# Kernel tuning notes

Hardware: AMD Instinct MI355X
Metric: run time of the kernel (lower is better)

Reference implementation:

```python
import jax, jax.numpy as jnp
import numpy as np

B, S, D = 4, 2048, 1024

def setup_inputs() -> dict:
    key = jax.random.key(0)
    kv, kk, kq, kw = jax.random.split(key, 4)
    scale = 1.0 / np.sqrt(D)
    v = jax.random.normal(kv, (B, S, D), dtype=jnp.float32)
    k = jax.random.normal(kk, (B, S, D), dtype=jnp.float32)
    q = jax.random.normal(kq, (B, S, D), dtype=jnp.float32)
    wi = jax.random.normal(kw, (D, D), dtype=jnp.float32) * scale
    mask = jnp.tril(jnp.ones((S, S), dtype=bool))[None, :, :]  # causal [1,S,S]
    return {"v": v, "k": k, "q": q, "wi": wi, "mask": mask}

def reference(v, k, q, wi, mask):
    # project q, k, v with the shared weight wi
    q = q @ wi
    k = k @ wi
    v = v @ wi
    # scaled dot-product scores [B,S,S]
    scores = jnp.einsum('bqd,bkd->bqk', q, k) / jnp.sqrt(jnp.asarray(q.shape[-1], q.dtype))
    scores = jnp.where(mask, scores, jnp.asarray(-1e10, scores.dtype))
    attn = jax.nn.softmax(scores, axis=-1)
    # residual: q + attn @ v
    return q + jnp.einsum('bqk,bkd->bqd', attn, v)
```

## Files before the change

### kernel.cpp

```cpp
#include <hip/hip_runtime.h>
#include <hip/hip_bf16.h>

typedef __hip_bfloat16 bf16;
typedef short bf16x8 __attribute__((ext_vector_type(8)));
typedef float f32x4 __attribute__((ext_vector_type(4)));

#define HT 16384

__device__ __forceinline__ void gload16(const void* g, void* l) {
    __builtin_amdgcn_global_load_lds(
        (const __attribute__((address_space(1))) void*)g,
        (__attribute__((address_space(3))) void*)l, 16, 0, 0);
}

__device__ __forceinline__ void stage_half(char* lds, const bf16* src, int ld,
                                           int rowbase, int k0, int slotIdx,
                                           int tid)
{
    char* dst = lds + (size_t)slotIdx * HT + tid * 16;
    const int sub = tid >> 3;
    const int cb  = ((tid & 7) ^ (sub & 7)) << 4;
    #pragma unroll
    for (int p = 0; p < 2; ++p) {
        const int row = p * 64 + sub;
        const char* g = (const char*)(src + (size_t)(rowbase + row) * ld + k0) + cb;
        gload16(g, dst + p * 8192);
    }
}

__device__ __forceinline__ void stage_q(char* lds, const bf16* src, int ld,
                                        int rowbase, int k0, int slotIdx,
                                        int tid)
{
    char* dst = lds + (size_t)slotIdx * HT + tid * 16;
    #pragma unroll
    for (int p = 0; p < 4; ++p) {
        const int s = p * 256 + tid;
        const int row = s >> 3;
        const int cb = ((s & 7) ^ (row & 7)) << 4;
        const char* g = (const char*)(src + (size_t)(rowbase + row) * ld + k0) + cb;
        gload16(g, dst + p * 4096);
    }
}

__device__ __forceinline__ bf16x8 ldsfrag(const char* lds, int slotIdx,
                                          int row, int ks, int cb0)
{
    return *(const bf16x8*)(lds + (size_t)slotIdx * HT
                            + row * 128 + (cb0 ^ (ks << 6)));
}

__device__ __forceinline__ float bf2f(short s) {
    union { float f; unsigned u; } c;
    c.u = ((unsigned)(unsigned short)s) << 16;
    return c.f;
}

#define MF8(n0)                                                               \
    _Pragma("unroll") for (int m = 0; m < 4; ++m)                             \
    _Pragma("unroll") for (int dn = 0; dn < 2; ++dn)                          \
    _Pragma("unroll") for (int ks = 0; ks < 2; ++ks)                          \
        acc[m][(n0)+dn] = __builtin_amdgcn_mfma_f32_16x16x32_bf16(            \
            af[m][ks], bv[(n0)+dn][ks], acc[m][(n0)+dn], 0, 0, 0);

#define GEMM256_BODY(A_, lda_, B_, ldb_, brow_, bcol_)                        \
    f32x4 acc[4][4] = {};                                                     \
    bf16x8 af[4][2], bv[4][2];                                                \
    stage_half(lds, A_, lda_, brow_,       0, 0, tid);                        \
    stage_half(lds, A_, lda_, brow_ + 128, 0, 1, tid);                        \
    stage_half(lds, B_, ldb_, bcol_,       0, 6, tid);                        \
    stage_half(lds, A_, lda_, brow_,      64, 2, tid);                        \
    stage_half(lds, A_, lda_, brow_ + 128,64, 3, tid);                        \
    stage_half(lds, B_, ldb_, bcol_,     64, 7, tid);                         \
    asm volatile("s_waitcnt vmcnt(6)" ::: "memory");                          \
    __builtin_amdgcn_s_barrier();                                             \
    for (int t = 0; t < 16; ++t) {                                            \
        const int aslot = (t % 3) * 2 + hA;                                   \
        const int bslot = 6 + (t & 1);                                        \
        const int a2    = ((t + 2) % 3) * 2;                                  \
        const int k2    = min(t + 2, 15) << 6;                                \
        _Pragma("unroll") for (int m = 0; m < 4; ++m)                         \
        _Pragma("unroll") for (int ks = 0; ks < 2; ++ks)                      \
            af[m][ks] = ldsfrag(lds, aslot, rA + m * 16 + fr, ks, cb0);       \
        _Pragma("unroll") for (int n = 0; n < 4; ++n)                         \
        _Pragma("unroll") for (int ks = 0; ks < 2; ++ks)                      \
            bv[n][ks] = ldsfrag(lds, bslot, rB + n * 16 + fr, ks, cb0);       \
        stage_half(lds, A_, lda_, brow_,       k2, a2,     tid);              \
        stage_half(lds, A_, lda_, brow_ + 128, k2, a2 + 1, tid);              \
        __builtin_amdgcn_s_barrier();                                         \
        __builtin_amdgcn_s_setprio(1);                                        \
        MF8(0)                                                                \
        __builtin_amdgcn_s_setprio(0);                                        \
        __builtin_amdgcn_s_barrier();                                         \
        stage_half(lds, B_, ldb_, bcol_, k2, bslot, tid);                     \
        __builtin_amdgcn_s_barrier();                                         \
        __builtin_amdgcn_s_setprio(1);                                        \
        MF8(2)                                                                \
        __builtin_amdgcn_s_setprio(0);                                        \
        asm volatile("s_waitcnt vmcnt(6)" ::: "memory");                      \
        __builtin_amdgcn_s_barrier();                                         \
    }

template<int MODE>
__launch_bounds__(512, 2)
__global__ void gemm_a256(const bf16* __restrict__ A, const bf16* __restrict__ B,
                          bf16* __restrict__ Cb, float* __restrict__ Cf)
{
    extern __shared__ char lds[];
    const int gx = gridDim.x;
    const int nwg = gx * gridDim.y;
    const int chunk = nwg >> 3;
    const int orig = blockIdx.y * gx + blockIdx.x;
    const int wk2 = (orig & 7) * chunk + (orig >> 3);
    const int bi = wk2 / gx, bj = wk2 % gx;
    const int brow = bi * 256, bcol = bj * 128;

    const int tid  = threadIdx.x;
    const int lane = tid & 63;
    const int w    = tid >> 6;
    const int wm   = w >> 1, wn = w & 1;
    const int fr   = lane & 15, fq = lane >> 4;
    const int cb0  = ((fr & 7) ^ fq) << 4;
    const int hA   = wm >> 1;
    const int rA   = (wm & 1) * 64;
    const int rB   = wn * 64;

    GEMM256_BODY(A, 1024, B, 1024, brow, bcol)

    #pragma unroll
    for (int mf = 0; mf < 4; ++mf) {
        const int r0 = brow + wm * 64 + mf * 16 + fq * 4;
        #pragma unroll
        for (int nf = 0; nf < 4; ++nf) {
            const int c = bcol + wn * 64 + nf * 16 + fr;
            #pragma unroll
            for (int j = 0; j < 4; ++j) {
                if (MODE == 0)
                    Cb[(size_t)(r0 + j) * 1024 + c] =
                        __float2bfloat16(acc[mf][nf][j]);
                else
                    Cf[(size_t)(r0 + j) * 1024 + c] = acc[mf][nf][j];
            }
        }
    }
}

__launch_bounds__(512, 1)
__global__ void scores8(const bf16* __restrict__ qG, const bf16* __restrict__ kb,
                        bf16* __restrict__ P)
{
    extern __shared__ char lds[];
    const int orig = blockIdx.y * 8 + blockIdx.x;
    const int wk2 = (orig & 7) * 18 + (orig >> 3);
    const int bz = wk2 / 36;
    const int j  = wk2 % 36;
    int bi = (int)((__fsqrt_rn(8.0f * j + 1.0f) - 1.0f) * 0.5f);
    while ((bi + 1) * (bi + 2) / 2 <= j) ++bi;
    while (bi * (bi + 1) / 2 > j) --bi;
    const int bj = j - bi * (bi + 1) / 2;
    const int brow = bi * 256, bcol = bj * 256;
    const bf16* A = qG + (size_t)bz * 2048 * 1024;
    const bf16* B = kb + (size_t)bz * 2048 * 1024;
    bf16* Cp = P + (size_t)bz * 2048 * 2048;

    const int tid  = threadIdx.x;
    const int lane = tid & 63;
    const int w    = tid >> 6;
    const int wm   = w >> 2;
    const int wn   = w & 3;
    const int bh   = wn >> 1;
    const int rBl  = (wn & 1) * 64;
    const int fr   = lane & 15, fq = lane >> 4;
    const int cb0  = ((fr & 7) ^ fq) << 4;

    f32x4 acc[8][4] = {};
    bf16x8 af0[4][2], af1[4][2], bv0[2][2], bv1[2][2];

#define AS(t,h) ((((t) % 3) * 2) + (h))
#define BS(t,h) (6 + (((t) & 1) * 2) + (h))

    stage_half(lds, A, 1024, brow,       0, AS(0,0), tid);
    stage_half(lds, A, 1024, brow + 128, 0, AS(0,1), tid);
    stage_half(lds, B, 1024, bcol,       0, BS(0,0), tid);
    stage_half(lds, B, 1024, bcol + 128, 0, BS(0,1), tid);
    stage_half(lds, A, 1024, brow,      64, AS(1,0), tid);
    stage_half(lds, A, 1024, brow + 128,64, AS(1,1), tid);
    stage_half(lds, B, 1024, bcol,     64, BS(1,0), tid);
    asm volatile("s_waitcnt vmcnt(6)" ::: "memory");
    __builtin_amdgcn_s_barrier();

#define MFQ(MH, NH, AF, BV)                                                   \
    _Pragma("unroll") for (int m = 0; m < 4; ++m)                             \
    _Pragma("unroll") for (int n = 0; n < 2; ++n)                             \
    _Pragma("unroll") for (int ks = 0; ks < 2; ++ks)                          \
        acc[(MH)*4+m][(NH)*2+n] = __builtin_amdgcn_mfma_f32_16x16x32_bf16(    \
            AF[m][ks], BV[n][ks], acc[(MH)*4+m][(NH)*2+n], 0, 0, 0);

    for (int t = 0; t < 16; ++t) {
        const int kN  = min(t + 1, 15) << 6;
        const int kNN = min(t + 2, 15) << 6;
        const int as  = AS(t, wm);
        const int bs2 = BS(t, bh);

        #pragma unroll
        for (int m = 0; m < 4; ++m)
            #pragma unroll
            for (int ks = 0; ks < 2; ++ks)
                af0[m][ks] = ldsfrag(lds, as, m * 16 + fr, ks, cb0);
        #pragma unroll
        for (int n = 0; n < 2; ++n)
            #pragma unroll
            for (int ks = 0; ks < 2; ++ks)
                bv0[n][ks] = ldsfrag(lds, bs2, rBl + n * 16 + fr, ks, cb0);
        stage_half(lds, B, 1024, bcol + 128, kN, BS(t + 1, 1), tid);
        __builtin_amdgcn_s_barrier();
        __builtin_amdgcn_s_setprio(1);
        MFQ(0, 0, af0, bv0)
        __builtin_amdgcn_s_setprio(0);
        __builtin_amdgcn_s_barrier();

        #pragma unroll
        for (int m = 0; m < 4; ++m)
            #pragma unroll
            for (int ks = 0; ks < 2; ++ks)
                af1[m][ks] = ldsfrag(lds, as, 64 + m * 16 + fr, ks, cb0);
        stage_half(lds, A, 1024, brow, kNN, AS(t + 2, 0), tid);
        __builtin_amdgcn_s_barrier();
        __builtin_amdgcn_s_setprio(1);
        MFQ(1, 0, af1, bv0)
        __builtin_amdgcn_s_setprio(0);
        __builtin_amdgcn_s_barrier();

        #pragma unroll
        for (int n = 0; n < 2; ++n)
            #pragma unroll
            for (int ks = 0; ks < 2; ++ks)
                bv1[n][ks] = ldsfrag(lds, bs2, rBl + 32 + n * 16 + fr, ks, cb0);
        stage_half(lds, A, 1024, brow + 128, kNN, AS(t + 2, 1), tid);
        __builtin_amdgcn_s_barrier();
        __builtin_amdgcn_s_setprio(1);
        MFQ(1, 1, af1, bv1)
        __builtin_amdgcn_s_setprio(0);
        __builtin_amdgcn_s_barrier();

        stage_half(lds, B, 1024, bcol, kNN, BS(t + 2, 0), tid);
        __builtin_amdgcn_s_barrier();
        __builtin_amdgcn_s_setprio(1);
        MFQ(0, 1, af0, bv1)
        __builtin_amdgcn_s_setprio(0);
        asm volatile("s_waitcnt vmcnt(6)" ::: "memory");
        __builtin_amdgcn_s_barrier();
    }
#undef MFQ
#undef AS
#undef BS

    #pragma unroll
    for (int mf = 0; mf < 8; ++mf) {
        const int r0 = brow + wm * 128 + mf * 16 + fq * 4;
        #pragma unroll
        for (int nf = 0; nf < 4; ++nf) {
            const int c = bcol + wn * 64 + nf * 16 + fr;
            #pragma unroll
            for (int jj = 0; jj < 4; ++jj)
                Cp[(size_t)(r0 + jj) * 2048 + c] =
                    __float2bfloat16(acc[mf][nf][jj] * 0.03125f);
        }
    }
}

__device__ __forceinline__ void tile128pv(char* lds, const bf16* A, const bf16* B,
                                          bf16* Cb, const bf16* Res,
                                          int lda, int ldb, int ldcb,
                                          int brow, int bcol, int NT, int tid)
{
    const int lane = tid & 63;
    const int w    = tid >> 6;
    const int wm   = w >> 1, wn = w & 1;
    const int fr   = lane & 15, fq = lane >> 4;
    const int cb0  = ((fr & 7) ^ fq) << 4;

    f32x4 acc[4][4] = {};
    bf16x8 af[4][2], bv[4][2];

    stage_q(lds, A, lda, brow, 0,  0, tid);
    stage_q(lds, B, ldb, bcol, 0,  3, tid);
    stage_q(lds, A, lda, brow, 64, 1, tid);
    stage_q(lds, B, ldb, bcol, 64, 4, tid);
    asm volatile("s_waitcnt vmcnt(8)" ::: "memory");
    __builtin_amdgcn_s_barrier();

    for (int t = 0; t < NT; ++t) {
        const int aslot = t % 3, bslot = 3 + (t & 1);
        const int k2 = min(t + 2, NT - 1) << 6;

        #pragma unroll
        for (int m = 0; m < 4; ++m)
            #pragma unroll
            for (int ks = 0; ks < 2; ++ks)
                af[m][ks] = ldsfrag(lds, aslot, wm * 64 + m * 16 + fr, ks, cb0);
        #pragma unroll
        for (int n = 0; n < 4; ++n)
            #pragma unroll
            for (int ks = 0; ks < 2; ++ks)
                bv[n][ks] = ldsfrag(lds, bslot, wn * 64 + n * 16 + fr, ks, cb0);
        stage_q(lds, A, lda, brow, k2, (t + 2) % 3, tid);
        __builtin_amdgcn_s_barrier();
        __builtin_amdgcn_s_setprio(1);
        #pragma unroll
        for (int m = 0; m < 4; ++m)
            #pragma unroll
            for (int n = 0; n < 2; ++n)
                #pragma unroll
                for (int ks = 0; ks < 2; ++ks)
                    acc[m][n] = __builtin_amdgcn_mfma_f32_16x16x32_bf16(
                        af[m][ks], bv[n][ks], acc[m][n], 0, 0, 0);
        __builtin_amdgcn_s_setprio(0);
        __builtin_amdgcn_s_barrier();

        stage_q(lds, B, ldb, bcol, k2, bslot, tid);
        __builtin_amdgcn_s_barrier();
        __builtin_amdgcn_s_setprio(1);
        #pragma unroll
        for (int m = 0; m < 4; ++m)
            #pragma unroll
            for (int n = 2; n < 4; ++n)
                #pragma unroll
                for (int ks = 0; ks < 2; ++ks)
                    acc[m][n] = __builtin_amdgcn_mfma_f32_16x16x32_bf16(
                        af[m][ks], bv[n][ks], acc[m][n], 0, 0, 0);
        __builtin_amdgcn_s_setprio(0);
        asm volatile("s_waitcnt vmcnt(8)" ::: "memory");
        __builtin_amdgcn_s_barrier();
    }

    #pragma unroll
    for (int mf = 0; mf < 4; ++mf) {
        const int r0 = brow + wm * 64 + mf * 16 + fq * 4;
        #pragma unroll
        for (int nf = 0; nf < 4; ++nf) {
            const int c = bcol + wn * 64 + nf * 16 + fr;
            #pragma unroll
            for (int j = 0; j < 4; ++j)
                Cb[(size_t)(r0 + j) * ldcb + c] = __float2bfloat16(
                    acc[mf][nf][j] +
                    __bfloat162float(Res[(size_t)(r0 + j) * ldcb + c]));
        }
    }
}

__launch_bounds__(256, 2)
__global__ void pv128(const bf16* __restrict__ P, const bf16* __restrict__ vT,
                      const bf16* __restrict__ qb, bf16* __restrict__ Y)
{
    extern __shared__ char lds[];
    const int x  = blockIdx.x;
    const int u  = x & 255;
    const int bs = u & 7;
    const int bj = (u >> 3) & 7;
    const int bz = u >> 6;
    const int bi = (x >> 8) ? (15 - bs) : bs;

    tile128pv(lds,
              P + (size_t)bz * 2048 * 2048,
              vT + (size_t)bz * 1024 * 2048,
              Y + (size_t)bz * 2048 * 1024,
              qb + (size_t)bz * 2048 * 1024,
              2048, 2048, 1024,
              bi * 128, bj * 128, 2 * (bi + 1), threadIdx.x);
}

__device__ __forceinline__ void tr64(const float* __restrict__ src, int ldsrc,
                                     bf16* __restrict__ dst, int lddst,
                                     int r0, int c0, int tid, bf16* tl)
{
    #pragma unroll
    for (int p = 0; p < 4; ++p) {
        const int rr = p * 16 + (tid >> 4);
        const int cc = (tid & 15) * 4;
        float4 x = *(const float4*)(src + (size_t)(r0 + rr) * ldsrc + c0 + cc);
        bf16* o = tl + rr * 66 + cc;
        o[0] = __float2bfloat16(x.x);
        o[1] = __float2bfloat16(x.y);
        o[2] = __float2bfloat16(x.z);
        o[3] = __float2bfloat16(x.w);
    }
    __syncthreads();
    #pragma unroll
    for (int p = 0; p < 2; ++p) {
        const int crow = p * 32 + (tid >> 3);
        const int sc   = (tid & 7) * 8;
        union { short h[8]; bf16x8 v8; } o;
        #pragma unroll
        for (int j = 0; j < 8; ++j) {
            bf16 hh = tl[(sc + j) * 66 + crow];
            o.h[j] = *(short*)&hh;
        }
        *(bf16x8*)(dst + (size_t)(c0 + crow) * lddst + r0 + sc) = o.v8;
    }
}

__global__ void prep(const float* __restrict__ q, const float* __restrict__ k,
                     const float* __restrict__ wi, const float* __restrict__ v,
                     bf16* __restrict__ qb, bf16* __restrict__ kb,
                     bf16* __restrict__ Wb, bf16* __restrict__ vT,
                     bf16* __restrict__ Wt)
{
    __shared__ bf16 tl[64 * 66];
    const int b = blockIdx.x;
    const int tid = threadIdx.x;
    if (b < 2048) {
        const int z = b >> 9, rem = b & 511;
        const int d0 = (rem >> 5) * 64, s0 = (rem & 31) * 64;
        tr64(v + (size_t)z * 2048 * 1024, 1024,
             vT + (size_t)z * 1024 * 2048, 2048, s0, d0, tid, tl);
    } else if (b < 2304) {
        const int t2 = b - 2048;
        const int n0 = (t2 & 15) * 64, k0 = (t2 >> 4) * 64;
        tr64(wi, 1024, Wt, 1024, k0, n0, tid, tl);
    } else {
        const int N8 = 8192 * 1024 / 8, W8 = 1024 * 1024 / 8;
        const int total = 2 * N8 + W8;
        const int nconv = gridDim.x - 2304;
        for (int i = (b - 2304) * 256 + tid; i < total; i += nconv * 256) {
            const float4* s;
            bf16* dst;
            int j;
            if (i < N8)          { s = (const float4*)q;  dst = qb; j = i; }
            else if (i < 2 * N8) { s = (const float4*)k;  dst = kb; j = i - N8; }
            else                 { s = (const float4*)wi; dst = Wb; j = i - 2 * N8; }
            float4 a = s[2 * j], bb = s[2 * j + 1];
            float vals[8] = {a.x, a.y, a.z, a.w, bb.x, bb.y, bb.z, bb.w};
            union { short h[8]; bf16x8 v8; } o;
            #pragma unroll
            for (int e = 0; e < 8; ++e) {
                bf16 hh = __float2bfloat16(vals[e]);
                o.h[e] = *(short*)&hh;
            }
            ((bf16x8*)dst)[j] = o.v8;
        }
    }
}

__launch_bounds__(256)
__global__ void softmax_rows(bf16* __restrict__ P)
{
    const int wid = threadIdx.x >> 6, lane = threadIdx.x & 63;
    const int r = blockIdx.x * 4 + wid, b = blockIdx.y;
    bf16* row = P + ((size_t)b * 2048 + r) * 2048;
    const int nv  = r + 1;
    const int rup = (r & ~127) + 128;

    float vals[4][8];
    float m = -1e30f;
    #pragma unroll
    for (int c = 0; c < 4; ++c) {
        const int k0 = c * 512 + lane * 8;
        if (k0 < rup) {
            bf16x8 x = *(const bf16x8*)(row + k0);
            #pragma unroll
            for (int j = 0; j < 8; ++j) {
                float f = (k0 + j < nv) ? bf2f(x[j]) : -1e30f;
                vals[c][j] = f;
                m = fmaxf(m, f);
            }
        } else {
            #pragma unroll
            for (int j = 0; j < 8; ++j) vals[c][j] = -1e30f;
        }
    }
    #pragma unroll
    for (int o = 32; o; o >>= 1) m = fmaxf(m, __shfl_xor(m, o));

    float sum = 0.f;
    #pragma unroll
    for (int c = 0; c < 4; ++c)
        #pragma unroll
        for (int j = 0; j < 8; ++j) {
            float e = __expf(vals[c][j] - m);
            vals[c][j] = e;
            sum += e;
        }
    #pragma unroll
    for (int o = 32; o; o >>= 1) sum += __shfl_xor(sum, o);
    const float inv = 1.0f / sum;

    #pragma unroll
    for (int c = 0; c < 4; ++c) {
        const int k0 = c * 512 + lane * 8;
        if (k0 < rup) {
            union { short h[8]; bf16x8 v8; } o;
            #pragma unroll
            for (int j = 0; j < 8; ++j) {
                bf16 hh = __float2bfloat16(vals[c][j] * inv);
                o.h[j] = *(short*)&hh;
            }
            *(bf16x8*)(row + k0) = o.v8;
        }
    }
}

extern "C" void kernel_launch(void* const* d_in, const int* in_sizes, int n_in,
                              void* d_out, int out_size, void* d_ws, size_t ws_size,
                              hipStream_t stream)
{
    const float* v  = (const float*)d_in[0];
    const float* k  = (const float*)d_in[1];
    const float* q  = (const float*)d_in[2];
    const float* wi = (const float*)d_in[3];
    float* out = (float*)d_out;

    char* ws = (char*)d_ws;
    const size_t MB = 1u << 20;
    bf16* Wb = (bf16*)(ws);
    bf16* Wt = (bf16*)(ws + 2 * MB);
    bf16* G  = (bf16*)(ws + 4 * MB);
    bf16* qb = (bf16*)(ws + 6 * MB);
    bf16* kb = (bf16*)(ws + 22 * MB);
    bf16* vT = (bf16*)(ws + 38 * MB);
    bf16* qG = (bf16*)(ws + 54 * MB);
    bf16* Y  = (bf16*)(ws + 70 * MB);
    bf16* P  = (bf16*)(ws + 86 * MB);

    (void)hipFuncSetAttribute((const void*)gemm_a256<0>,
            hipFuncAttributeMaxDynamicSharedMemorySize, 131072);
    (void)hipFuncSetAttribute((const void*)gemm_a256<2>,
            hipFuncAttributeMaxDynamicSharedMemorySize, 131072);
    (void)hipFuncSetAttribute((const void*)scores8,
            hipFuncAttributeMaxDynamicSharedMemorySize, 163840);
    (void)hipFuncSetAttribute((const void*)pv128,
            hipFuncAttributeMaxDynamicSharedMemorySize, 81920);

    prep<<<5376, 256, 0, stream>>>(q, k, wi, v, qb, kb, Wb, vT, Wt);

    gemm_a256<0><<<dim3(8, 4), 512, 131072, stream>>>(Wb, Wb, G, nullptr);

    gemm_a256<0><<<dim3(8, 32), 512, 131072, stream>>>(qb, G, qG, nullptr);

    scores8<<<dim3(8, 18), 512, 163840, stream>>>(qG, kb, P);

    softmax_rows<<<dim3(512, 4), 256, 0, stream>>>(P);

    pv128<<<dim3(512), 256, 81920, stream>>>(P, vT, qb, Y);

    gemm_a256<2><<<dim3(8, 32), 512, 131072, stream>>>(Y, Wt, nullptr, out);
}
```

Before: 160.9 us.

## Store transposed V in contiguous 128x64 tiles for PV staging

```diff
diff --git a/kernel.cpp b/kernel.cpp
--- a/kernel.cpp
+++ b/kernel.cpp
@@ -39,6 +39,21 @@
         const int row = s >> 3;
         const int cb = ((s & 7) ^ (row & 7)) << 4;
         const char* g = (const char*)(src + (size_t)(rowbase + row) * ld + k0) + cb;
+        gload16(g, dst + p * 4096);
+    }
+}
+
+__device__ __forceinline__ void stage_qt(char* lds, const bf16* vtz,
+                                         int bcol, int k0, int slotIdx, int tid)
+{
+    const bf16* tile = vtz + ((size_t)(bcol >> 7) * 32 + (k0 >> 6)) * 8192;
+    char* dst = lds + (size_t)slotIdx * HT + tid * 16;
+    #pragma unroll
+    for (int p = 0; p < 4; ++p) {
+        const int s = p * 256 + tid;
+        const int row = s >> 3;
+        const int cb = ((s & 7) ^ (row & 7)) << 4;
+        const char* g = (const char*)(tile + row * 64) + cb;
         gload16(g, dst + p * 4096);
     }
 }
@@ -269,9 +284,10 @@
     }
 }
 
-__device__ __forceinline__ void tile128pv(char* lds, const bf16* A, const bf16* B,
+__device__ __forceinline__ void tile128pv(char* lds, const bf16* A,
+                                          const bf16* vtz,
                                           bf16* Cb, const bf16* Res,
-                                          int lda, int ldb, int ldcb,
+                                          int lda, int ldcb,
                                           int brow, int bcol, int NT, int tid)
 {
     const int lane = tid & 63;
@@ -284,9 +300,9 @@
     bf16x8 af[4][2], bv[4][2];
 
     stage_q(lds, A, lda, brow, 0,  0, tid);
-    stage_q(lds, B, ldb, bcol, 0,  3, tid);
+    stage_qt(lds, vtz, bcol, 0,  3, tid);
     stage_q(lds, A, lda, brow, 64, 1, tid);
-    stage_q(lds, B, ldb, bcol, 64, 4, tid);
+    stage_qt(lds, vtz, bcol, 64, 4, tid);
     asm volatile("s_waitcnt vmcnt(8)" ::: "memory");
     __builtin_amdgcn_s_barrier();
 
@@ -318,7 +334,7 @@
         __builtin_amdgcn_s_setprio(0);
         __builtin_amdgcn_s_barrier();
 
-        stage_q(lds, B, ldb, bcol, k2, bslot, tid);
+        stage_qt(lds, vtz, bcol, k2, bslot, tid);
         __builtin_amdgcn_s_barrier();
         __builtin_amdgcn_s_setprio(1);
         #pragma unroll
@@ -363,10 +379,10 @@
 
     tile128pv(lds,
               P + (size_t)bz * 2048 * 2048,
-              vT + (size_t)bz * 1024 * 2048,
+              vT + (size_t)bz * 8 * 32 * 8192,
               Y + (size_t)bz * 2048 * 1024,
               qb + (size_t)bz * 2048 * 1024,
-              2048, 2048, 1024,
+              2048, 1024,
               bi * 128, bj * 128, 2 * (bi + 1), threadIdx.x);
 }
 
@@ -406,23 +422,50 @@
                      bf16* __restrict__ Wb, bf16* __restrict__ vT,
                      bf16* __restrict__ Wt)
 {
-    __shared__ bf16 tl[64 * 66];
+    __shared__ bf16 tls[128 * 66];
     const int b = blockIdx.x;
     const int tid = threadIdx.x;
-    if (b < 2048) {
-        const int z = b >> 9, rem = b & 511;
-        const int d0 = (rem >> 5) * 64, s0 = (rem & 31) * 64;
-        tr64(v + (size_t)z * 2048 * 1024, 1024,
-             vT + (size_t)z * 1024 * 2048, 2048, s0, d0, tid, tl);
-    } else if (b < 2304) {
-        const int t2 = b - 2048;
+    if (b < 1024) {
+        const int z = b >> 8, rem = b & 255;
+        const int dt = rem >> 5, st = rem & 31;
+        const float* vz = v + (size_t)z * 2048 * 1024;
+        bf16* tile = vT + (((size_t)z * 8 + dt) * 32 + st) * 8192;
+
+        #pragma unroll
+        for (int p = 0; p < 8; ++p) {
+            const int fid = p * 256 + tid;
+            const int srow = fid >> 5;
+            const int d0 = (fid & 31) * 4;
+            float4 x = *(const float4*)(vz + (size_t)(st * 64 + srow) * 1024
+                                        + dt * 128 + d0);
+            tls[(d0 + 0) * 66 + srow] = __float2bfloat16(x.x);
+            tls[(d0 + 1) * 66 + srow] = __float2bfloat16(x.y);
+            tls[(d0 + 2) * 66 + srow] = __float2bfloat16(x.z);
+            tls[(d0 + 3) * 66 + srow] = __float2bfloat16(x.w);
+        }
+        __syncthreads();
+
+        const int d  = tid >> 1;
+        const int sh = (tid & 1) * 32;
+        #pragma unroll
+        for (int jj = 0; jj < 4; ++jj) {
+            union { short h[8]; bf16x8 v8; } o;
+            #pragma unroll
+            for (int e = 0; e < 8; ++e) {
+                bf16 hh = tls[d * 66 + sh + jj * 8 + e];
+                o.h[e] = *(short*)&hh;
+            }
+            *(bf16x8*)(tile + (size_t)d * 64 + sh + jj * 8) = o.v8;
+        }
+    } else if (b < 1280) {
+        const int t2 = b - 1024;
         const int n0 = (t2 & 15) * 64, k0 = (t2 >> 4) * 64;
-        tr64(wi, 1024, Wt, 1024, k0, n0, tid, tl);
+        tr64(wi, 1024, Wt, 1024, k0, n0, tid, tls);
     } else {
         const int N8 = 8192 * 1024 / 8, W8 = 1024 * 1024 / 8;
         const int total = 2 * N8 + W8;
-        const int nconv = gridDim.x - 2304;
-        for (int i = (b - 2304) * 256 + tid; i < total; i += nconv * 256) {
+        const int nconv = gridDim.x - 1280;
+        for (int i = (b - 1280) * 256 + tid; i < total; i += nconv * 256) {
             const float4* s;
             bf16* dst;
             int j;
@@ -531,7 +574,7 @@
     (void)hipFuncSetAttribute((const void*)pv128,
             hipFuncAttributeMaxDynamicSharedMemorySize, 81920);
 
-    prep<<<5376, 256, 0, stream>>>(q, k, wi, v, qb, kb, Wb, vT, Wt);
+    prep<<<4352, 256, 0, stream>>>(q, k, wi, v, qb, kb, Wb, vT, Wt);
 
     gemm_a256<0><<<dim3(8, 4), 512, 131072, stream>>>(Wb, Wb, G, nullptr);
 
```

After: 164.8 us. 1.02x slower.
